# Optimization experiments

Measured on AMD Instinct MI355X. Metric: run time of the kernel, lower is better.

## Reference

```python
import jax, jax.numpy as jnp
import numpy as np

EPS = 1e-5
HD = 16          # hidden_dim
OC = 256         # out_chs
NH = 8           # num_heads (groups of qkv conv)
DV = OC // (2 * HD)  # per-head value dim = 8


def conv_bn_silu(x, w, gamma, beta, mean, var, stride=1, pad=1, groups=1):
    # Conv2d(bias=False) + BatchNorm2d(eval) + SiLU, NCHW/OIHW
    y = jax.lax.conv_general_dilated(
        x, w, (stride, stride), [(pad, pad), (pad, pad)],
        dimension_numbers=('NCHW', 'OIHW', 'NCHW'),
        feature_group_count=groups)
    inv = gamma * jax.lax.rsqrt(var + EPS)
    y = y * inv[None, :, None, None] + (beta - mean * inv)[None, :, None, None]
    return y * jax.nn.sigmoid(y)


def _bn_params(key, c):
    k1, k2, k3, k4 = jax.random.split(key, 4)
    g = 1.0 + 0.1 * jax.random.normal(k1, (c,), jnp.float32)
    b = 0.1 * jax.random.normal(k2, (c,), jnp.float32)
    m = 0.1 * jax.random.normal(k3, (c,), jnp.float32)
    v = jax.random.uniform(k4, (c,), jnp.float32, 0.5, 1.5)
    return g, b, m, v


def setup_inputs() -> dict:
    key = jax.random.key(0)
    ks = jax.random.split(key, 8)
    B, C, H, W = 16, 256, 80, 80
    qkv_out = HD * 2 + OC // 2  # 160
    d = {}
    d['x'] = jax.random.normal(ks[0], (B, C, H, W), jnp.float32)
    # qkv_conv: grouped 3x3, groups=NH -> in per group = C//NH
    d['qkv_w'] = jax.random.normal(ks[1], (qkv_out, C // NH, 3, 3), jnp.float32) * 0.05
    d['qkv_g'], d['qkv_b'], d['qkv_m'], d['qkv_v'] = _bn_params(ks[2], qkv_out)
    # hidden_conv: dense 3x3
    d['hid_w'] = jax.random.normal(ks[3], (OC, C, 3, 3), jnp.float32) * 0.02
    d['hid_g'], d['hid_b'], d['hid_m'], d['hid_v'] = _bn_params(ks[4], OC)
    # out_conv: 1x1 on (OC//2*3) channels
    d['out_w'] = jax.random.normal(ks[5], (OC, OC // 2 * 3, 1, 1), jnp.float32) * 0.05
    d['out_g'], d['out_b'], d['out_m'], d['out_v'] = _bn_params(ks[6], OC)
    return d


def reference(x, qkv_w, qkv_g, qkv_b, qkv_m, qkv_v,
              hid_w, hid_g, hid_b, hid_m, hid_v,
              out_w, out_g, out_b, out_m, out_v):
    B, C, H, W = x.shape
    N = H * W
    qkv = conv_bn_silu(x, qkv_w, qkv_g, qkv_b, qkv_m, qkv_v, stride=1, pad=1, groups=NH)
    q = qkv[:, :HD]               # (B, HD, H, W)
    k = qkv[:, HD:2 * HD]
    v = qkv[:, 2 * HD:]           # (B, OC//2, H, W)
    # permute to (B, N, HD) / (B, N, HD, DV), channel-major reshape matches torch .view
    q = q.transpose(0, 2, 3, 1).reshape(B, N, HD)
    k = k.transpose(0, 2, 3, 1).reshape(B, N, HD)
    v = v.transpose(0, 2, 3, 1).reshape(B, N, HD, DV)
    # per-pixel tiny attention: attn[b,n,i,j] = softmax_j(q_i * k_j)
    attn = jax.nn.softmax(q[..., :, None] * k[..., None, :], axis=-1)  # (B,N,HD,HD)
    y = jnp.einsum('bnij,bnjd->bnid', attn, v)                          # (B,N,HD,DV)
    # torch: permute(0,2,3,1).view(B, OC//2, H, W)
    y = y.transpose(0, 2, 3, 1).reshape(B, OC // 2, H, W)
    h = conv_bn_silu(x, hid_w, hid_g, hid_b, hid_m, hid_v, stride=1, pad=1)
    y = jnp.concatenate([y, h], axis=1)  # (B, OC//2*3, H, W)
    return conv_bn_silu(y, out_w, out_g, out_b, out_m, out_v, stride=1, pad=0)
```

## Files before the change

### kernel.cpp

```cpp
#include <hip/hip_runtime.h>
#include <stdint.h>

typedef unsigned short u16;
typedef unsigned int u32;
typedef __attribute__((ext_vector_type(4))) float f32x4;
typedef __attribute__((ext_vector_type(8))) __bf16 bf16x8;

#define EPS_BN 1e-5f

__device__ __forceinline__ u16 f2bf(float f) {
  u32 u = __builtin_bit_cast(u32, f);
  u32 r = (u + 0x7fffu + ((u >> 16) & 1u)) >> 16;
  return (u16)r;
}

__device__ __forceinline__ float silu_f(float v) {
  return v / (1.0f + __expf(-v));
}

__device__ __forceinline__ void gll16(const void* g, void* l) {
  __builtin_amdgcn_global_load_lds(
      (__attribute__((address_space(1))) void*)(void*)g,
      (__attribute__((address_space(3))) void*)l, 16, 0, 0);
}

__global__ __launch_bounds__(256) void prep(
    const float* __restrict__ qkv_w, const float* __restrict__ qg,
    const float* __restrict__ qb, const float* __restrict__ qm,
    const float* __restrict__ qv,
    const float* __restrict__ hid_w, const float* __restrict__ hg,
    const float* __restrict__ hb, const float* __restrict__ hm,
    const float* __restrict__ hv,
    const float* __restrict__ out_w, const float* __restrict__ og,
    const float* __restrict__ ob, const float* __restrict__ om,
    const float* __restrict__ ov,
    u16* __restrict__ wtb, u16* __restrict__ w2b, u16* __restrict__ wqp,
    float* __restrict__ bnq_s, float* __restrict__ bnq_b,
    float* __restrict__ bnh_s, float* __restrict__ bnh_b,
    float* __restrict__ bn2s, float* __restrict__ bn2b,
    float* __restrict__ zpg)
{
  const int gid = blockIdx.x * 256 + threadIdx.x;
  if (gid < 256 * 2304) {
    int j = gid / 2304, k = gid - j * 2304;
    int tap = k >> 8, c = k & 255;
    wtb[gid] = f2bf(hid_w[(j * 256 + c) * 9 + tap]);
  }
  if (gid < 73728) {
    int g = gid / 9216;
    int r = gid - g * 9216;
    int j = r / 288, k = r - j * 288;
    int tap = k >> 5, cg = k & 31;
    float v = 0.f;
    if (j < 20) v = qkv_w[((g * 20 + j) * 32 + cg) * 9 + tap];
    wqp[gid] = f2bf(v);
  }
  if (gid < 98304) w2b[gid] = f2bf(out_w[gid]);
  if (gid < 160) {
    float iv = qg[gid] * rsqrtf(qv[gid] + EPS_BN);
    bnq_s[gid] = iv; bnq_b[gid] = qb[gid] - qm[gid] * iv;
  }
  if (gid < 256) {
    float iv = hg[gid] * rsqrtf(hv[gid] + EPS_BN);
    bnh_s[gid] = iv; bnh_b[gid] = hb[gid] - hm[gid] * iv;
    float iv2 = og[gid] * rsqrtf(ov[gid] + EPS_BN);
    bn2s[gid] = iv2; bn2b[gid] = ob[gid] - om[gid] * iv2;
  }
  if (gid < 64) zpg[gid] = 0.f;
}

__global__ __launch_bounds__(256) void nchw2nhwc(
    const float* __restrict__ x, u16* __restrict__ xn)
{
  __shared__ u16 T[80 * 66];
  const int t = threadIdx.x;
  const int ct = blockIdx.x;
  const int h  = blockIdx.y;
  const int b  = blockIdx.z;
  const float* src = x + ((size_t)b * 256 + ct * 64) * 6400 + h * 80;
  for (int it = 0; it < 5; ++it) {
    int idx = it * 256 + t;
    int cl = idx / 20, w4 = idx - cl * 20;
    float4 v = *(const float4*)(src + (size_t)cl * 6400 + w4 * 4);
    T[(w4 * 4 + 0) * 66 + cl] = f2bf(v.x);
    T[(w4 * 4 + 1) * 66 + cl] = f2bf(v.y);
    T[(w4 * 4 + 2) * 66 + cl] = f2bf(v.z);
    T[(w4 * 4 + 3) * 66 + cl] = f2bf(v.w);
  }
  __syncthreads();
  u16* dst = xn + ((size_t)(b * 80 + h) * 80) * 256 + ct * 64;
  for (int it = 0; it < 5; ++it) {
    int idx = it * 256 + t;
    int wl = idx >> 4;
    int cl = (idx & 15) * 4;
    ushort4 v4;
    v4.x = T[wl * 66 + cl + 0];
    v4.y = T[wl * 66 + cl + 1];
    v4.z = T[wl * 66 + cl + 2];
    v4.w = T[wl * 66 + cl + 3];
    *(ushort4*)(dst + (size_t)wl * 256 + cl) = v4;
  }
}

__global__ __launch_bounds__(512, 4) void gemm_main(
    const u16* __restrict__ xn, const u16* __restrict__ wt,
    const float* __restrict__ bns, const float* __restrict__ bnb,
    const float* __restrict__ zpg, u16* __restrict__ ycat)
{
  __shared__ __attribute__((aligned(16))) u16 Al[128 * 64];
  __shared__ __attribute__((aligned(16))) u16 Bl[256 * 64];
  const int t = threadIdx.x;
  const int wave = t >> 6, lane = t & 63;
  const int wm = wave >> 2;
  const int wn = wave & 3;
  const int orig = blockIdx.x;
  const int wg = (orig & 7) * 100 + (orig >> 3);
  const int ptile = wg * 128;

  const int srcc = (((lane & 7) ^ ((lane >> 3) & 7)) * 8);
  const int c16 = lane & 15, lq = lane >> 4;

  int pbA[2], hhA[2], wwA[2];
#pragma unroll
  for (int l = 0; l < 2; ++l) {
    int row = wave * 8 + (lane >> 3) + l * 64;
    int p = ptile + row;
    pbA[l] = p;
    int hw = p % 6400;
    hhA[l] = hw / 80;
    wwA[l] = hw - (hw / 80) * 80;
  }
  int bofB[4];
#pragma unroll
  for (int l = 0; l < 4; ++l) {
    int row = wave * 8 + (lane >> 3) + l * 64;
    bofB[l] = row * 2304 + srcc;
  }

  f32x4 acc[4][4];
#pragma unroll
  for (int m = 0; m < 4; ++m)
#pragma unroll
    for (int n = 0; n < 4; ++n) {
      f32x4 z = {0.f, 0.f, 0.f, 0.f};
      acc[m][n] = z;
    }

  for (int ks = 0; ks < 36; ++ks) {
    const int k0 = ks * 64;
    const int tap = ks >> 2;
    const int c0 = (ks & 3) * 64;
    const int dh = tap / 3 - 1, dw = tap - (tap / 3) * 3 - 1;
    const int dp = dh * 80 + dw;
    __syncthreads();
#pragma unroll
    for (int l = 0; l < 2; ++l) {
      bool ok = ((unsigned)(hhA[l] + dh) < 80u) & ((unsigned)(wwA[l] + dw) < 80u);
      const u16* src = ok
          ? (xn + ((size_t)(pbA[l] + dp) * 256 + c0 + srcc))
          : (const u16*)zpg;
      gll16(src, Al + (wave * 8 + l * 64) * 64);
    }
#pragma unroll
    for (int l = 0; l < 4; ++l)
      gll16(wt + (size_t)(bofB[l] + k0), Bl + (wave * 8 + l * 64) * 64);
    __syncthreads();
#pragma unroll
    for (int kk = 0; kk < 2; ++kk) {
      const int q = kk * 4 + lq;
      bf16x8 av[4], bv[4];
#pragma unroll
      for (int m = 0; m < 4; ++m) {
        int r = wm * 64 + m * 16 + c16;
        av[m] = *(const bf16x8*)(Al + r * 64 + (q ^ (r & 7)) * 8);
      }
#pragma unroll
      for (int n = 0; n < 4; ++n) {
        int j = wn * 64 + n * 16 + c16;
        bv[n] = *(const bf16x8*)(Bl + j * 64 + (q ^ (j & 7)) * 8);
      }
#pragma unroll
      for (int m = 0; m < 4; ++m)
#pragma unroll
        for (int n = 0; n < 4; ++n)
          acc[m][n] = __builtin_amdgcn_mfma_f32_16x16x32_bf16(
              av[m], bv[n], acc[m][n], 0, 0, 0);
    }
  }

  const int rg = lq;
#pragma unroll
  for (int n = 0; n < 4; ++n) {
    int j = wn * 64 + n * 16 + c16;
    float sc = bns[j], bi = bnb[j];
#pragma unroll
    for (int m = 0; m < 4; ++m) {
      int p0 = ptile + wm * 64 + m * 16 + rg * 4;
#pragma unroll
      for (int r = 0; r < 4; ++r) {
        float v = silu_f(acc[m][n][r] * sc + bi);
        ycat[(size_t)(p0 + r) * 384 + 128 + j] = f2bf(v);
      }
    }
  }
}

__global__ __launch_bounds__(256, 3) void qkv_attn(
    const u16* __restrict__ xn, const u16* __restrict__ wqp,
    const float* __restrict__ bnq_s, const float* __restrict__ bnq_b,
    u16* __restrict__ ycat)
{
  __shared__ __attribute__((aligned(16))) char LB[40960];
  u16* HB = (u16*)LB;
  float* qs = (float*)LB;

  const int t = threadIdx.x;
  const int wave = t >> 6, lane = t & 63;
  const int orig = blockIdx.x;
  const int wg = (orig & 7) * 100 + (orig >> 3);
  const int ptile = wg * 128;
  const int pbase = ptile - 88;

  const int srcc = (((lane & 7) ^ ((lane >> 3) & 7)) * 8);
  const int q = lane >> 4, c16 = lane & 15;

  int ph[2], pw[2];
#pragma unroll
  for (int m = 0; m < 2; ++m) {
    int p = ptile + wave * 32 + m * 16 + c16;
    int hw = p % 6400;
    ph[m] = hw / 80;
    pw[m] = hw - (hw / 80) * 80;
  }

  auto STAGE_H = [&](int cc) {
#pragma unroll
    for (int r = 0; r < 10; ++r) {
      int row = r * 32 + wave * 8 + (lane >> 3);
      int p = pbase + row;
      int pc = p < 0 ? 0 : (p > 102399 ? 102399 : p);
      gll16(xn + (size_t)pc * 256 + cc * 64 + srcc,
            HB + (r * 32 + wave * 8) * 64);
    }
  };

  bf16x8 zv;
#pragma unroll
  for (int i = 0; i < 8; ++i) zv[i] = (__bf16)0.0f;

  f32x4 acc[2][16];
#pragma unroll
  for (int m = 0; m < 2; ++m)
#pragma unroll
    for (int f = 0; f < 16; ++f) {
      f32x4 z = {0.f, 0.f, 0.f, 0.f};
      acc[m][f] = z;
    }

#pragma unroll
  for (int cc = 0; cc < 4; ++cc) {
    __syncthreads();
    STAGE_H(cc);
    __syncthreads();
    for (int tap = 0; tap < 9; ++tap) {
      const int dh = tap / 3 - 1, dw = tap - (tap / 3) * 3 - 1;
      const int dp = dh * 80 + dw;
      bf16x8 bq[2][2];
#pragma unroll
      for (int h = 0; h < 2; ++h)
#pragma unroll
        for (int nf = 0; nf < 2; ++nf) {
          int row = (2 * cc + h) * 32 + nf * 16 + c16;
          bq[h][nf] =
              *(const bf16x8*)(wqp + (size_t)row * 288 + tap * 32 + q * 8);
        }
      bf16x8 av[2][2];
#pragma unroll
      for (int m = 0; m < 2; ++m) {
        int rl = wave * 32 + m * 16 + c16 + 88 + dp;
        bool ok = ((unsigned)(ph[m] + dh) < 80u) &
                  ((unsigned)(pw[m] + dw) < 80u);
#pragma unroll
        for (int h = 0; h < 2; ++h) {
          int q8 = h * 4 + q;
          bf16x8 raw = *(const bf16x8*)(HB + rl * 64 + ((q8 ^ (rl & 7)) * 8));
          av[m][h] = ok ? raw : zv;
        }
      }
#pragma unroll
      for (int h = 0; h < 2; ++h)
#pragma unroll
        for (int m = 0; m < 2; ++m)
#pragma unroll
          for (int nf = 0; nf < 2; ++nf)
            acc[m][(2 * cc + h) * 2 + nf] = __builtin_amdgcn_mfma_f32_16x16x32_bf16(
                av[m][h], bq[h][nf], acc[m][(2 * cc + h) * 2 + nf], 0, 0, 0);
    }
  }

  __syncthreads();

#pragma unroll
  for (int hf = 0; hf < 2; ++hf) {
    if ((wave >> 1) == hf) {
#pragma unroll
      for (int f = 0; f < 16; ++f) {
        int jj = (f & 1) * 16 + c16;
        if (jj >= 20) continue;
        int oc = (f >> 1) * 20 + jj;
        float sc = bnq_s[oc], bi = bnq_b[oc];
#pragma unroll
        for (int m = 0; m < 2; ++m) {
          int pl0 = (wave & 1) * 32 + m * 16 + q * 4;
#pragma unroll
          for (int r = 0; r < 4; ++r)
            qs[(pl0 + r) * 160 + oc] = silu_f(acc[m][f][r] * sc + bi);
        }
      }
    }
    __syncthreads();
    for (int it = 0; it < 4; ++it) {
      int idx = it * 256 + t;
      int pxl = idx >> 4, i = idx & 15;
      const float* row = qs + pxl * 160;
      const float qi = row[i];
      float s[16];
      float mx = -3.4e38f;
#pragma unroll
      for (int j = 0; j < 16; ++j) { s[j] = qi * row[16 + j]; mx = fmaxf(mx, s[j]); }
      float sum = 0.f;
#pragma unroll
      for (int j = 0; j < 16; ++j) { s[j] = __expf(s[j] - mx); sum += s[j]; }
      const float inv = 1.0f / sum;
      float y[8];
#pragma unroll
      for (int d = 0; d < 8; ++d) y[d] = 0.f;
#pragma unroll
      for (int j = 0; j < 16; ++j) {
        const float a = s[j];
        const float* vr = row + 32 + j * 8;
#pragma unroll
        for (int d = 0; d < 8; ++d) y[d] += a * vr[d];
      }
      union { u16 u[8]; uint4 v4; } pk;
#pragma unroll
      for (int d = 0; d < 8; ++d) pk.u[d] = f2bf(y[d] * inv);
      *(uint4*)(ycat + (size_t)(ptile + hf * 64 + pxl) * 384 + i * 8) = pk.v4;
    }
    __syncthreads();
  }
}

__global__ __launch_bounds__(256, 2) void gemm_out(
    const u16* __restrict__ w2, const u16* __restrict__ ycat,
    const float* __restrict__ bns, const float* __restrict__ bnb,
    float* __restrict__ out)
{
  __shared__ __attribute__((aligned(16))) u16 Al[128 * 64];
  __shared__ __attribute__((aligned(16))) u16 Bl[128 * 64];
  const int t = threadIdx.x;
  const int wave = t >> 6, lane = t & 63;
  const int wr = wave >> 1, wc = wave & 1;
  const int orig = blockIdx.y * 2 + blockIdx.x;
  const int wg = (orig & 7) * 200 + (orig >> 3);
  const int octile = (wg / 800) * 128;
  const int ptile = (wg % 800) * 128;

  const int srcc = (((lane & 7) ^ ((lane >> 3) & 7)) * 8);
  int bofA[4], bofB[4];
#pragma unroll
  for (int c = 0; c < 4; ++c) {
    int m = wave * 32 + c * 8 + (lane >> 3);
    bofA[c] = (octile + m) * 384 + srcc;
    bofB[c] = (ptile + m) * 384 + srcc;
  }
  u16* AlW = Al + wave * 2048;
  u16* BlW = Bl + wave * 2048;

  f32x4 acc[4][4];
#pragma unroll
  for (int m = 0; m < 4; ++m)
#pragma unroll
    for (int n = 0; n < 4; ++n) {
      f32x4 z = {0.f, 0.f, 0.f, 0.f};
      acc[m][n] = z;
    }

  for (int ks = 0; ks < 6; ++ks) {
    const int k0 = ks * 64;
    __syncthreads();
#pragma unroll
    for (int c = 0; c < 4; ++c) gll16(w2 + (size_t)(bofA[c] + k0), AlW + c * 512);
#pragma unroll
    for (int c = 0; c < 4; ++c) gll16(ycat + (size_t)(bofB[c] + k0), BlW + c * 512);
    __syncthreads();
#pragma unroll
    for (int kk = 0; kk < 2; ++kk) {
      const int q = kk * 4 + (lane >> 4);
      const int c16 = lane & 15;
      bf16x8 av[4], bv[4];
#pragma unroll
      for (int m = 0; m < 4; ++m) {
        int r = wr * 64 + m * 16 + c16;
        av[m] = *(const bf16x8*)(Al + r * 64 + (q ^ (r & 7)) * 8);
      }
#pragma unroll
      for (int n = 0; n < 4; ++n) {
        int r = wc * 64 + n * 16 + c16;
        bv[n] = *(const bf16x8*)(Bl + r * 64 + (q ^ (r & 7)) * 8);
      }
#pragma unroll
      for (int m = 0; m < 4; ++m)
#pragma unroll
        for (int n = 0; n < 4; ++n)
          acc[m][n] = __builtin_amdgcn_mfma_f32_16x16x32_bf16(
              av[m], bv[n], acc[m][n], 0, 0, 0);
    }
  }

  const int c16 = lane & 15, rg = lane >> 4;
  const int b = ptile / 6400;
  const int hwb = ptile - b * 6400;
#pragma unroll
  for (int m = 0; m < 4; ++m) {
    int oc0 = octile + wr * 64 + m * 16 + rg * 4;
#pragma unroll
    for (int n = 0; n < 4; ++n) {
      int hw = hwb + wc * 64 + n * 16 + c16;
#pragma unroll
      for (int r = 0; r < 4; ++r) {
        int oc = oc0 + r;
        float v = silu_f(acc[m][n][r] * bns[oc] + bnb[oc]);
        out[((size_t)b * 256 + oc) * 6400 + hw] = v;
      }
    }
  }
}

extern "C" void kernel_launch(void* const* d_in, const int* in_sizes, int n_in,
                              void* d_out, int out_size, void* d_ws, size_t ws_size,
                              hipStream_t stream) {
  (void)in_sizes; (void)n_in; (void)out_size; (void)ws_size;
  const float* x    = (const float*)d_in[0];
  const float* qkvw = (const float*)d_in[1];
  const float* qg   = (const float*)d_in[2];
  const float* qb   = (const float*)d_in[3];
  const float* qm   = (const float*)d_in[4];
  const float* qv   = (const float*)d_in[5];
  const float* hw_  = (const float*)d_in[6];
  const float* hg   = (const float*)d_in[7];
  const float* hb   = (const float*)d_in[8];
  const float* hm   = (const float*)d_in[9];
  const float* hv   = (const float*)d_in[10];
  const float* ow   = (const float*)d_in[11];
  const float* og   = (const float*)d_in[12];
  const float* ob   = (const float*)d_in[13];
  const float* om   = (const float*)d_in[14];
  const float* ov   = (const float*)d_in[15];

  char* ws = (char*)d_ws;
  float* zpg   = (float*)(ws + 0);
  float* bnq_s = (float*)(ws + 256);
  float* bnq_b = (float*)(ws + 1280);
  float* bnh_s = (float*)(ws + 2304);
  float* bnh_b = (float*)(ws + 3328);
  float* bn2s  = (float*)(ws + 4352);
  float* bn2b  = (float*)(ws + 5376);
  u16*   wtb   = (u16*)(ws + 6400);
  u16*   w2b   = (u16*)(ws + 1186048);
  u16*   wqp   = (u16*)(ws + 1382656);
  u16*   xn    = (u16*)(ws + 1536000);
  u16*   ycat  = (u16*)(ws + 119500800);
  float* out   = (float*)d_out;

  prep<<<dim3(2304), dim3(256), 0, stream>>>(
      qkvw, qg, qb, qm, qv, hw_, hg, hb, hm, hv, ow, og, ob, om, ov,
      wtb, w2b, wqp, bnq_s, bnq_b, bnh_s, bnh_b, bn2s, bn2b, zpg);
  nchw2nhwc<<<dim3(4, 80, 16), dim3(256), 0, stream>>>(x, xn);
  gemm_main<<<dim3(800), dim3(512), 0, stream>>>(
      xn, wtb, bnh_s, bnh_b, zpg, ycat);
  qkv_attn<<<dim3(800), dim3(256), 0, stream>>>(
      xn, wqp, bnq_s, bnq_b, ycat);
  gemm_out<<<dim3(2, 800), dim3(256), 0, stream>>>(
      w2b, ycat, bn2s, bn2b, out);
}
```

Measured before the change: 336.9 us.

## Double-buffer qkv_attn halo staging and run attention epilogue in a single pass

The qkv_attn kernel now keeps two LDS halo buffers, so the global-to-LDS load for the next channel chunk is issued while MFMAs run on the current one. This hides load latency and drops one barrier per chunk. The larger LDS footprint also lets the epilogue write all 128 pixels' q/k/v into LDS at once and run the softmax-attention in one pass instead of two halves. In exchange, occupancy drops from 3 to 2 blocks per CU because LDS use doubles.

```diff
diff --git a/kernel.cpp b/kernel.cpp
--- a/kernel.cpp
+++ b/kernel.cpp
@@ -205,13 +205,14 @@
   }
 }
 
-__global__ __launch_bounds__(256, 3) void qkv_attn(
+__global__ __launch_bounds__(256, 2) void qkv_attn(
     const u16* __restrict__ xn, const u16* __restrict__ wqp,
     const float* __restrict__ bnq_s, const float* __restrict__ bnq_b,
     u16* __restrict__ ycat)
 {
-  __shared__ __attribute__((aligned(16))) char LB[40960];
-  u16* HB = (u16*)LB;
+  __shared__ __attribute__((aligned(16))) char LB[81920];
+  u16* HB0 = (u16*)LB;
+  u16* HB1 = (u16*)(LB + 40960);
   float* qs = (float*)LB;
 
   const int t = threadIdx.x;
@@ -233,14 +234,14 @@
     pw[m] = hw - (hw / 80) * 80;
   }
 
-  auto STAGE_H = [&](int cc) {
+  auto STAGE_H = [&](int cc, u16* dst) {
 #pragma unroll
     for (int r = 0; r < 10; ++r) {
       int row = r * 32 + wave * 8 + (lane >> 3);
       int p = pbase + row;
       int pc = p < 0 ? 0 : (p > 102399 ? 102399 : p);
       gll16(xn + (size_t)pc * 256 + cc * 64 + srcc,
-            HB + (r * 32 + wave * 8) * 64);
+            dst + (r * 32 + wave * 8) * 64);
     }
   };
 
@@ -257,11 +258,16 @@
       acc[m][f] = z;
     }
 
+  STAGE_H(0, HB0);
+  asm volatile("s_waitcnt vmcnt(0)" ::: "memory");
+  __builtin_amdgcn_sched_barrier(0);
+  __syncthreads();
+
 #pragma unroll
   for (int cc = 0; cc < 4; ++cc) {
-    __syncthreads();
-    STAGE_H(cc);
-    __syncthreads();
+    const u16* HBc = (cc & 1) ? HB1 : HB0;
+    u16* HBn = (cc & 1) ? HB0 : HB1;
+    if (cc < 3) STAGE_H(cc + 1, HBn);
     for (int tap = 0; tap < 9; ++tap) {
       const int dh = tap / 3 - 1, dw = tap - (tap / 3) * 3 - 1;
       const int dp = dh * 80 + dw;
@@ -283,7 +289,7 @@
 #pragma unroll
         for (int h = 0; h < 2; ++h) {
           int q8 = h * 4 + q;
-          bf16x8 raw = *(const bf16x8*)(HB + rl * 64 + ((q8 ^ (rl & 7)) * 8));
+          bf16x8 raw = *(const bf16x8*)(HBc + rl * 64 + ((q8 ^ (rl & 7)) * 8));
           av[m][h] = ok ? raw : zv;
         }
       }
@@ -296,58 +302,60 @@
             acc[m][(2 * cc + h) * 2 + nf] = __builtin_amdgcn_mfma_f32_16x16x32_bf16(
                 av[m][h], bq[h][nf], acc[m][(2 * cc + h) * 2 + nf], 0, 0, 0);
     }
-  }
-
+    if (cc < 3) {
+      asm volatile("s_waitcnt vmcnt(0)" ::: "memory");
+      __builtin_amdgcn_sched_barrier(0);
+      __syncthreads();
+    }
+  }
+
+  asm volatile("s_waitcnt vmcnt(0)" ::: "memory");
+  __builtin_amdgcn_sched_barrier(0);
   __syncthreads();
 
 #pragma unroll
-  for (int hf = 0; hf < 2; ++hf) {
-    if ((wave >> 1) == hf) {
-#pragma unroll
-      for (int f = 0; f < 16; ++f) {
-        int jj = (f & 1) * 16 + c16;
-        if (jj >= 20) continue;
-        int oc = (f >> 1) * 20 + jj;
-        float sc = bnq_s[oc], bi = bnq_b[oc];
-#pragma unroll
-        for (int m = 0; m < 2; ++m) {
-          int pl0 = (wave & 1) * 32 + m * 16 + q * 4;
-#pragma unroll
-          for (int r = 0; r < 4; ++r)
-            qs[(pl0 + r) * 160 + oc] = silu_f(acc[m][f][r] * sc + bi);
-        }
-      }
-    }
-    __syncthreads();
-    for (int it = 0; it < 4; ++it) {
-      int idx = it * 256 + t;
-      int pxl = idx >> 4, i = idx & 15;
-      const float* row = qs + pxl * 160;
-      const float qi = row[i];
-      float s[16];
-      float mx = -3.4e38f;
-#pragma unroll
-      for (int j = 0; j < 16; ++j) { s[j] = qi * row[16 + j]; mx = fmaxf(mx, s[j]); }
-      float sum = 0.f;
-#pragma unroll
-      for (int j = 0; j < 16; ++j) { s[j] = __expf(s[j] - mx); sum += s[j]; }
-      const float inv = 1.0f / sum;
-      float y[8];
-#pragma unroll
-      for (int d = 0; d < 8; ++d) y[d] = 0.f;
-#pragma unroll
-      for (int j = 0; j < 16; ++j) {
-        const float a = s[j];
-        const float* vr = row + 32 + j * 8;
-#pragma unroll
-        for (int d = 0; d < 8; ++d) y[d] += a * vr[d];
-      }
-      union { u16 u[8]; uint4 v4; } pk;
-#pragma unroll
-      for (int d = 0; d < 8; ++d) pk.u[d] = f2bf(y[d] * inv);
-      *(uint4*)(ycat + (size_t)(ptile + hf * 64 + pxl) * 384 + i * 8) = pk.v4;
-    }
-    __syncthreads();
+  for (int f = 0; f < 16; ++f) {
+    int jj = (f & 1) * 16 + c16;
+    if (jj >= 20) continue;
+    int oc = (f >> 1) * 20 + jj;
+    float sc = bnq_s[oc], bi = bnq_b[oc];
+#pragma unroll
+    for (int m = 0; m < 2; ++m) {
+      int pl0 = wave * 32 + m * 16 + q * 4;
+#pragma unroll
+      for (int r = 0; r < 4; ++r)
+        qs[(pl0 + r) * 160 + oc] = silu_f(acc[m][f][r] * sc + bi);
+    }
+  }
+  __syncthreads();
+
+  for (int it = 0; it < 8; ++it) {
+    int idx = it * 256 + t;
+    int px = idx >> 4, i = idx & 15;
+    const float* row = qs + px * 160;
+    const float qi = row[i];
+    float s[16];
+    float mx = -3.4e38f;
+#pragma unroll
+    for (int j = 0; j < 16; ++j) { s[j] = qi * row[16 + j]; mx = fmaxf(mx, s[j]); }
+    float sum = 0.f;
+#pragma unroll
+    for (int j = 0; j < 16; ++j) { s[j] = __expf(s[j] - mx); sum += s[j]; }
+    const float inv = 1.0f / sum;
+    float y[8];
+#pragma unroll
+    for (int d = 0; d < 8; ++d) y[d] = 0.f;
+#pragma unroll
+    for (int j = 0; j < 16; ++j) {
+      const float a = s[j];
+      const float* vr = row + 32 + j * 8;
+#pragma unroll
+      for (int d = 0; d < 8; ++d) y[d] += a * vr[d];
+    }
+    union { u16 u[8]; uint4 v4; } pk;
+#pragma unroll
+    for (int d = 0; d < 8; ++d) pk.u[d] = f2bf(y[d] * inv);
+    *(uint4*)(ycat + (size_t)(ptile + px) * 384 + i * 8) = pk.v4;
   }
 }
 
```

Result: faster. 302.4 us (-10.2%).
